# Performance work log

Measured on AMD Instinct MI355X. Metric: run time of the kernel, lower is better.

Reference implementation:

```python
import jax, jax.numpy as jnp
import numpy as np

NUM_CLASSES = 21
EPS = 1e-6
MOMENTUM = 0.99
K_WEAK = 16
K_STRONG = 256
PROB_THRESH = 0.95
IGNORE = 255
NEG = -1e30


def _normalize(x, axis=-1):
    # matches F.normalize(p=2) / CosineSimilarity with eps=1e-6
    n = jnp.linalg.norm(x, axis=axis, keepdims=True)
    return x / jnp.maximum(n, EPS)


def setup_inputs() -> dict:
    key = jax.random.key(0)
    k0, k1, k2, k3, k4, k5 = jax.random.split(key, 6)
    B, C, H, W = 8, 256, 128, 128
    feature_weak = jax.random.normal(k0, (B, C, H, W), jnp.float32)
    feature_strong = jax.random.normal(k1, (B, C, H, W), jnp.float32)
    probablity_weak = jax.random.uniform(k2, (B, H, W), jnp.float32)
    memory_bank = jax.random.normal(k3, (NUM_CLASSES, 1, C), jnp.float32)
    pred_weak = jax.random.randint(k4, (B, H, W), 0, NUM_CLASSES)
    ignore_mask = jax.random.randint(k5, (B, H, W), 0, 256)
    return {
        'feature_weak': feature_weak,
        'feature_strong': feature_strong,
        'probablity_weak': probablity_weak,
        'memory_bank': memory_bank,
        'pred_weak': pred_weak,
        'ignore_mask': ignore_mask,
    }


def reference(feature_weak, feature_strong, probablity_weak, memory_bank, pred_weak, ignore_mask):
    B, C, H, W = feature_weak.shape
    N = B * H * W
    fw = feature_weak.transpose(0, 2, 3, 1).reshape(N, C)   # weak pixel feats
    fs = feature_strong.transpose(0, 2, 3, 1).reshape(N, C) # strong pixel feats
    seg = pred_weak.reshape(N)
    ign = ignore_mask.reshape(N)  # same-size bilinear resize (align_corners) is identity
    prob = probablity_weak.reshape(N)

    valid = ign != IGNORE
    conf = valid & (prob > PROB_THRESH)

    cls = jnp.arange(NUM_CLASSES)
    is_cls = seg[None, :] == cls[:, None]        # [K, N]
    m_weak = is_cls & conf[None, :]              # per-class high-confidence mask
    m_strong = is_cls & valid[None, :]
    n_weak = m_weak.sum(axis=1)                  # [K]
    n_strong = m_strong.sum(axis=1)

    protos = memory_bank[:, 0, :]                # [K, C]
    pn = _normalize(protos)
    sim_w = _normalize(fw) @ pn.T                # [N, K] cos(pixel_weak, proto)
    sim_s = _normalize(fs) @ pn.T                # [N, K] cos(pixel_strong, proto)

    sw = jnp.where(m_weak, sim_w.T, NEG)         # [K, N]
    ss = jnp.where(m_strong, -sim_s.T, NEG)      # negate -> bottom-k via top_k
    _, idx_w = jax.lax.top_k(sw, K_WEAK)         # [K, 16] most-similar weak pixels
    _, idx_s = jax.lax.top_k(ss, K_STRONG)       # [K, 256] least-similar strong pixels

    # select_feature duplicates the top element: slots are ranks [0,0,1,...,14]
    ranks = jnp.maximum(jnp.arange(K_WEAK) - 1, 0)
    sel_w = fw[idx_w[:, ranks]]                  # [K, 16, C]
    sel_s = fs[idx_s]                            # [K, 256, C]

    kw = jnp.minimum(K_WEAK, n_weak)
    ks = jnp.minimum(K_STRONG, n_strong)
    valid_w = jnp.arange(K_WEAK)[None, :] < kw[:, None]     # [K, 16]
    valid_s = jnp.arange(K_STRONG)[None, :] < ks[:, None]   # [K, 256]

    # calculate_loss: weak side detached, max over strong dim, sum / strong count
    wn = _normalize(jax.lax.stop_gradient(sel_w))
    sn = _normalize(sel_s)
    cosm = jnp.einsum('kwc,ksc->kws', wn, sn)    # [K, 16, 256]
    cosm = jnp.where(valid_s[:, None, :], cosm, NEG)
    max_sim = jnp.where(valid_w, cosm.max(axis=2), 0.0)     # [K, 16]
    class_ok = (n_weak > 0) & (n_strong > 0)
    sim_sum = jnp.where(class_ok, max_sim.sum(axis=1), 0.0).sum()
    count = jnp.where(class_ok, ks, 0).sum()
    loss = jnp.where(count > 0, 1.0 - sim_sum / count, 0.0)

    # update_memory: per-class mean of high-confidence weak feats, EMA scatter
    fw_ng = jax.lax.stop_gradient(fw)            # .data copy -> no grad
    wsum = m_weak.astype(fw.dtype) @ fw_ng       # [K, C] segmented sum
    mean = wsum / jnp.maximum(n_weak, 1).astype(fw.dtype)[:, None]
    new_protos = jnp.where((n_weak > 0)[:, None],
                           MOMENTUM * protos + (1.0 - MOMENTUM) * mean,
                           protos)
    new_memory_bank = new_protos[:, None, :]     # [K, 1, C]
    return loss, new_memory_bank
```

## Files before the change

kernel.cpp:

```cpp
#include <hip/hip_runtime.h>
#include <stdint.h>

#define NCLS  21
#define CDIM  256
#define HWSZ  16384
#define NPIX  131072
#define EPSV  1e-6f
#define NEGV  -1e30f
#define CAP_W 4096
#define CAP_S 16384
#define KSEL  256
#define NCC   8
#define CCH   (CDIM/NCC)
#define NPART 8
#define NBLK  (NPIX/1024)

__device__ __forceinline__ uint64_t pack_key(float v, unsigned idx) {
  unsigned u = __float_as_uint(v);
  u = (u & 0x80000000u) ? ~u : (u | 0x80000000u);
  return ((uint64_t)(~u) << 32) | (uint64_t)idx;
}

__global__ void k0_init(const float* __restrict__ mb, float* pn, float* wsum) {
  int k = blockIdx.x, t = threadIdx.x;
  float v = mb[k * CDIM + t];
  float s = v * v;
  for (int o = 32; o > 0; o >>= 1) s += __shfl_down(s, o, 64);
  __shared__ float wsh[4];
  int wid = t >> 6, lane = t & 63;
  if (lane == 0) wsh[wid] = s;
  __syncthreads();
  float tot = wsh[0] + wsh[1] + wsh[2] + wsh[3];
  float inv = 1.0f / fmaxf(sqrtf(tot), EPSV);
  pn[k * CDIM + t] = v * inv;
  wsum[k * CDIM + t] = 0.0f;
}

__global__ void k1a_stream(const float* __restrict__ fw, const float* __restrict__ fs,
                           const float* __restrict__ prob, const int* __restrict__ seg,
                           const int* __restrict__ ign, const float* __restrict__ pn,
                           float* part, float* wsum, int* cnts) {
  __shared__ float pnT[CCH * NCLS];
  __shared__ float wloc[NCLS * (CCH + 1)];
  __shared__ int hs[NCLS], hw2[NCLS];
  int t = threadIdx.x;
  int pg = blockIdx.x;
  int cc = blockIdx.y;
  int c0 = cc * CCH;
  for (int i = t; i < CCH * NCLS; i += 256) {
    int c = i / NCLS, k = i % NCLS;
    pnT[i] = pn[k * CDIM + c0 + c];
  }
  for (int i = t; i < NCLS * (CCH + 1); i += 256) wloc[i] = 0.0f;
  if (cc == 0) {
    for (int i = t; i < NCLS; i += 256) { hs[i] = 0; hw2[i] = 0; }
  }
  __syncthreads();

  int n0 = pg * 1024 + t * 4;
  int b = n0 >> 14, hw = n0 & (HWSZ - 1);
  int4   sg = *(const int4*)(seg + n0);
  int4   ig = *(const int4*)(ign + n0);
  float4 pr = *(const float4*)(prob + n0);
  bool v0 = (ig.x != 255), v1 = (ig.y != 255), v2 = (ig.z != 255), v3 = (ig.w != 255);
  bool cf0 = v0 && (pr.x > 0.95f);
  bool cf1 = v1 && (pr.y > 0.95f);
  bool cf2 = v2 && (pr.z > 0.95f);
  bool cf3 = v3 && (pr.w > 0.95f);
  if (cc == 0) {
    if (v0) atomicAdd(&hs[sg.x], 1);
    if (v1) atomicAdd(&hs[sg.y], 1);
    if (v2) atomicAdd(&hs[sg.z], 1);
    if (v3) atomicAdd(&hs[sg.w], 1);
    if (cf0) atomicAdd(&hw2[sg.x], 1);
    if (cf1) atomicAdd(&hw2[sg.y], 1);
    if (cf2) atomicAdd(&hw2[sg.z], 1);
    if (cf3) atomicAdd(&hw2[sg.w], 1);
  }

  const float* fwp = fw + ((size_t)b * CDIM + c0) * HWSZ + hw;
  const float* fsp = fs + ((size_t)b * CDIM + c0) * HWSZ + hw;

  float4 dw = {0,0,0,0}, nw = {0,0,0,0}, dsv = {0,0,0,0}, ns = {0,0,0,0};
#pragma unroll 4
  for (int cl = 0; cl < CCH; ++cl) {
    float4 a = *(const float4*)(fwp + (size_t)cl * HWSZ);
    float4 s = *(const float4*)(fsp + (size_t)cl * HWSZ);
    float p0 = pnT[cl * NCLS + sg.x];
    float p1 = pnT[cl * NCLS + sg.y];
    float p2 = pnT[cl * NCLS + sg.z];
    float p3 = pnT[cl * NCLS + sg.w];
    dw.x = fmaf(a.x, p0, dw.x); nw.x = fmaf(a.x, a.x, nw.x);
    dw.y = fmaf(a.y, p1, dw.y); nw.y = fmaf(a.y, a.y, nw.y);
    dw.z = fmaf(a.z, p2, dw.z); nw.z = fmaf(a.z, a.z, nw.z);
    dw.w = fmaf(a.w, p3, dw.w); nw.w = fmaf(a.w, a.w, nw.w);
    dsv.x = fmaf(s.x, p0, dsv.x); ns.x = fmaf(s.x, s.x, ns.x);
    dsv.y = fmaf(s.y, p1, dsv.y); ns.y = fmaf(s.y, s.y, ns.y);
    dsv.z = fmaf(s.z, p2, dsv.z); ns.z = fmaf(s.z, s.z, ns.z);
    dsv.w = fmaf(s.w, p3, dsv.w); ns.w = fmaf(s.w, s.w, ns.w);
    if (cf0) atomicAdd(&wloc[sg.x * (CCH + 1) + cl], a.x);
    if (cf1) atomicAdd(&wloc[sg.y * (CCH + 1) + cl], a.y);
    if (cf2) atomicAdd(&wloc[sg.z * (CCH + 1) + cl], a.z);
    if (cf3) atomicAdd(&wloc[sg.w * (CCH + 1) + cl], a.w);
  }
  float4* pp = (float4*)part + ((size_t)cc * NPIX + n0);
  pp[0] = make_float4(dw.x, nw.x, dsv.x, ns.x);
  pp[1] = make_float4(dw.y, nw.y, dsv.y, ns.y);
  pp[2] = make_float4(dw.z, nw.z, dsv.z, ns.z);
  pp[3] = make_float4(dw.w, nw.w, dsv.w, ns.w);

  __syncthreads();
  for (int i = t; i < NCLS * CCH; i += 256) {
    int k = i / CCH, cl = i % CCH;
    float v = wloc[k * (CCH + 1) + cl];
    if (v != 0.0f) atomicAdd(&wsum[k * CDIM + c0 + cl], v);
  }
  if (cc == 0) {
    for (int i = t; i < NCLS; i += 256) {
      cnts[pg * NCLS + i] = hs[i];
      cnts[NBLK * NCLS + pg * NCLS + i] = hw2[i];
    }
  }
}

__global__ void ks_scan(const int* __restrict__ cnts, int* offs, int* scnt, int* wcnt) {
  __shared__ int L[2 * NBLK * NCLS];
  int t = threadIdx.x;
  for (int i = t; i < 2 * NBLK * NCLS; i += 256) L[i] = cnts[i];
  __syncthreads();
  if (t < 2 * NCLS) {
    int q = t % NCLS;
    int typ = t / NCLS;
    int base = typ * NBLK * NCLS;
    int run = 0;
    for (int b2 = 0; b2 < NBLK; ++b2) {
      int v = L[base + b2 * NCLS + q];
      L[base + b2 * NCLS + q] = run;
      run += v;
    }
    if (typ == 0) scnt[q] = run; else wcnt[q] = run;
  }
  __syncthreads();
  for (int i = t; i < 2 * NBLK * NCLS; i += 256) offs[i] = L[i];
}

__global__ void k1b_write(const float* __restrict__ part, const float* __restrict__ prob,
                          const int* __restrict__ seg, const int* __restrict__ ign,
                          const int* __restrict__ offs, uint64_t* wkeys, uint64_t* skeys) {
  __shared__ int ls[NCLS], lw[NCLS];
  int t = threadIdx.x, pg = blockIdx.x;
  if (t < NCLS) {
    ls[t] = offs[pg * NCLS + t];
    lw[t] = offs[NBLK * NCLS + pg * NCLS + t];
  }
  __syncthreads();
  int n0 = pg * 1024 + t * 4;
  int4   sg = *(const int4*)(seg + n0);
  int4   ig = *(const int4*)(ign + n0);
  float4 pr = *(const float4*)(prob + n0);
  float dw[4] = {0,0,0,0}, nw[4] = {0,0,0,0}, ds[4] = {0,0,0,0}, ns[4] = {0,0,0,0};
#pragma unroll
  for (int cc = 0; cc < NCC; ++cc) {
    const float4* pp = (const float4*)part + ((size_t)cc * NPIX + n0);
#pragma unroll
    for (int i = 0; i < 4; ++i) {
      float4 v = pp[i];
      dw[i] += v.x; nw[i] += v.y; ds[i] += v.z; ns[i] += v.w;
    }
  }
  int   sga[4] = {sg.x, sg.y, sg.z, sg.w};
  int   iga[4] = {ig.x, ig.y, ig.z, ig.w};
  float pra[4] = {pr.x, pr.y, pr.z, pr.w};
#pragma unroll
  for (int i = 0; i < 4; ++i) {
    if (iga[i] != 255) {
      int q = sga[i];
      float sim_s = ds[i] / fmaxf(sqrtf(ns[i]), EPSV);
      int pos = atomicAdd(&ls[q], 1);
      if (pos < CAP_S) skeys[(size_t)q * CAP_S + pos] = pack_key(-sim_s, (unsigned)(n0 + i));
      if (pra[i] > 0.95f) {
        float sim_w = dw[i] / fmaxf(sqrtf(nw[i]), EPSV);
        int pw = atomicAdd(&lw[q], 1);
        if (pw < CAP_W) wkeys[(size_t)q * CAP_W + pw] = pack_key(sim_w, (unsigned)(n0 + i));
      }
    }
  }
}

__device__ void select_topk(const uint64_t* __restrict__ list, int cnt,
                            uint64_t* T, uint64_t* P, int* pcnt, int* woff) {
  int t = threadIdx.x;
  T[t] = ~0ull;
  if (t == 0) *pcnt = 0;
  __syncthreads();
  for (int base = 0; base < cnt; base += 256) {
    uint64_t key = (base + t < cnt) ? list[base + t] : ~0ull;
    uint64_t cutoff = T[KSEL - 1];
    bool pred = key < cutoff;
    unsigned long long mask = __ballot(pred);
    int wid = t >> 6, lane = t & 63;
    if (lane == 0) woff[wid] = __popcll(mask);
    int prefix = __popcll(mask & ((1ull << lane) - 1ull));
    __syncthreads();
    int off = 0;
    for (int w2 = 0; w2 < wid; ++w2) off += woff[w2];
    int total = woff[0] + woff[1] + woff[2] + woff[3];
    int old = *pcnt;
    if (pred) P[old + off + prefix] = key;
    int newc = old + total;
    __syncthreads();
    if (t == 0) *pcnt = newc;
    bool last = (base + 256 >= cnt);
    if (newc >= KSEL || (last && newc > 0)) {
      for (int i2 = t; i2 < 2 * KSEL; i2 += 256)
        if (i2 >= newc) P[i2] = ~0ull;
      for (unsigned size = 2; size <= 2 * KSEL; size <<= 1) {
        for (unsigned stride = size >> 1; stride > 0; stride >>= 1) {
          __syncthreads();
          unsigned lo = stride - 1;
          unsigned i = (((unsigned)t & ~lo) << 1) | ((unsigned)t & lo);
          unsigned j = i | stride;
          uint64_t a = P[i], b = P[j];
          bool up = ((i & size) == 0);
          if ((a > b) == up) { P[i] = b; P[j] = a; }
        }
      }
      __syncthreads();
      uint64_t a = T[t], b = P[KSEL - 1 - t];
      T[t] = a < b ? a : b;
      for (unsigned stride = KSEL / 2; stride > 0; stride >>= 1) {
        __syncthreads();
        if (((unsigned)t & stride) == 0) {
          uint64_t x = T[t], y = T[t + stride];
          if (x > y) { T[t] = y; T[t + stride] = x; }
        }
      }
      __syncthreads();
      if (t == 0) *pcnt = 0;
      __syncthreads();
    } else {
      __syncthreads();
    }
  }
}

__global__ void k2_topk(const uint64_t* __restrict__ wkeys, const uint64_t* __restrict__ skeys,
                        const int* wcnt, const int* scnt,
                        uint64_t* psel, int* idxw, int* kwv, int* nwv) {
  __shared__ uint64_t T[KSEL];
  __shared__ uint64_t P[2 * KSEL];
  __shared__ int pcnt;
  __shared__ int woff[4];
  int bid = blockIdx.x, t = threadIdx.x;
  if (bid < NCLS * NPART) {
    int k = bid / NPART, p = bid % NPART;
    int cnt = min(scnt[k], CAP_S);
    int chunk = (cnt + NPART - 1) / NPART;
    int lo = p * chunk;
    int hi = min(lo + chunk, cnt);
    int c = hi > lo ? hi - lo : 0;
    select_topk(skeys + (size_t)k * CAP_S + lo, c, T, P, &pcnt, woff);
    psel[((size_t)k * NPART + p) * KSEL + t] = T[t];
  } else {
    int k = bid - NCLS * NPART;
    int cnt_total = wcnt[k];
    int cnt = min(cnt_total, CAP_W);
    select_topk(wkeys + (size_t)k * CAP_W, cnt, T, P, &pcnt, woff);
    if (t < 16) idxw[k * 16 + t] = (int)(unsigned)(T[t] & 0xFFFFFFFFull);
    if (t == 0) { nwv[k] = cnt_total; kwv[k] = min(cnt_total, 16); }
  }
}

__global__ void k2m_merge(const uint64_t* __restrict__ psel, const int* scnt,
                          int* idxs, int* ksv, int* nsv) {
  int k = blockIdx.x, t = threadIdx.x;
  __shared__ uint64_t M[NPART * KSEL];
  for (int i = t; i < NPART * KSEL; i += 256) M[i] = psel[(size_t)k * NPART * KSEL + i];
  for (unsigned size = 2; size <= NPART * KSEL; size <<= 1) {
    for (unsigned stride = size >> 1; stride > 0; stride >>= 1) {
      __syncthreads();
      for (unsigned q = t; q < NPART * KSEL / 2; q += 256) {
        unsigned lo = stride - 1;
        unsigned i = ((q & ~lo) << 1) | (q & lo);
        unsigned j = i | stride;
        uint64_t a = M[i], b = M[j];
        bool up = ((i & size) == 0);
        if ((a > b) == up) { M[i] = b; M[j] = a; }
      }
    }
  }
  __syncthreads();
  idxs[k * KSEL + t] = (int)(unsigned)(M[t] & 0xFFFFFFFFull);
  if (t == 0) { int c = scnt[k]; nsv[k] = c; ksv[k] = c < KSEL ? c : KSEL; }
}

__global__ void k3a_gather(const float* __restrict__ fw, const float* __restrict__ fs,
                           const int* __restrict__ idxw, const int* __restrict__ idxs,
                           const int* __restrict__ kwv, const int* __restrict__ ksv,
                           float* dw_dense, float* ds_dense) {
  int k = blockIdx.y;
  int slot = blockIdx.x;
  int t = threadIdx.x;
  bool strong = slot < KSEL;
  float v = 0.0f;
  int n = 0;
  bool ok;
  if (strong) {
    ok = slot < ksv[k];
    if (ok) n = idxs[k * KSEL + slot];
  } else {
    int i = slot - KSEL;
    ok = i < kwv[k];
    int rank = i > 0 ? i - 1 : 0;
    if (ok) n = idxw[k * 16 + rank];
  }
  if (ok) {
    int b = n >> 14, hw = n & (HWSZ - 1);
    const float* f = strong ? fs : fw;
    v = f[(size_t)(b * CDIM + t) * HWSZ + hw];
  }
  float s = v * v;
  for (int o = 32; o > 0; o >>= 1) s += __shfl_down(s, o, 64);
  __shared__ float wsh[4];
  int wid = t >> 6, lane = t & 63;
  if (lane == 0) wsh[wid] = s;
  __syncthreads();
  float tot = wsh[0] + wsh[1] + wsh[2] + wsh[3];
  float inv = 1.0f / fmaxf(sqrtf(tot), EPSV);
  float out = v * inv;
  if (strong) ds_dense[((size_t)k * KSEL + slot) * CDIM + t] = out;
  else        dw_dense[((size_t)k * 16 + (slot - KSEL)) * CDIM + t] = out;
}

__global__ void k3b_loss(const float* __restrict__ dw_dense, const float* __restrict__ ds_dense,
                         const int* kwv, const int* ksv, const int* nwv, const int* nsv,
                         float* simsum, int* countk) {
  int k = blockIdx.x, t = threadIdx.x;
  int wid = t >> 6, lane = t & 63;
  __shared__ float wn[16 * CDIM];
  __shared__ float wred[4][16];
  for (int i = t; i < 16 * CDIM; i += 256) wn[i] = dw_dense[(size_t)k * 16 * CDIM + i];
  __syncthreads();
  int ks_ = ksv[k], kw_ = kwv[k];
  bool ok = (nwv[k] > 0) && (nsv[k] > 0);
  float dots[16];
#pragma unroll
  for (int i = 0; i < 16; ++i) dots[i] = 0.0f;
  bool jv = ok && (t < ks_);
  if (jv) {
    const float4* sp = (const float4*)(ds_dense + ((size_t)k * KSEL + t) * CDIM);
    for (int c4 = 0; c4 < CDIM / 4; ++c4) {
      float4 v = sp[c4];
#pragma unroll
      for (int i = 0; i < 16; ++i) {
        float4 w = ((const float4*)(wn + i * CDIM))[c4];
        dots[i] = fmaf(v.x, w.x, dots[i]);
        dots[i] = fmaf(v.y, w.y, dots[i]);
        dots[i] = fmaf(v.z, w.z, dots[i]);
        dots[i] = fmaf(v.w, w.w, dots[i]);
      }
    }
  }
#pragma unroll
  for (int i = 0; i < 16; ++i) {
    float v = jv ? dots[i] : NEGV;
    for (int o = 32; o > 0; o >>= 1) v = fmaxf(v, __shfl_down(v, o, 64));
    if (lane == 0) wred[wid][i] = v;
  }
  __syncthreads();
  if (t == 0) {
    float csum = 0.0f;
    for (int i = 0; i < kw_; ++i) {
      float m = fmaxf(fmaxf(wred[0][i], wred[1][i]), fmaxf(wred[2][i], wred[3][i]));
      csum += m;
    }
    simsum[k] = ok ? csum : 0.0f;
    countk[k] = ok ? ks_ : 0;
  }
}

__global__ void k4_final(const float* __restrict__ mb, const float* __restrict__ wsum,
                         const int* __restrict__ nwv, const float* __restrict__ simsum,
                         const int* __restrict__ countk, float* out) {
  int k = blockIdx.x, t = threadIdx.x;
  float p = mb[k * CDIM + t];
  float o = p;
  int nw = nwv[k];
  if (nw > 0) {
    float mean = wsum[k * CDIM + t] / (float)nw;
    o = 0.99f * p + 0.01f * mean;
  }
  out[1 + k * CDIM + t] = o;
  if (k == 0 && t == 0) {
    float ss = 0.0f;
    int cc = 0;
    for (int q = 0; q < NCLS; ++q) { ss += simsum[q]; cc += countk[q]; }
    out[0] = (cc > 0) ? (1.0f - ss / (float)cc) : 0.0f;
  }
}

extern "C" void kernel_launch(void* const* d_in, const int* in_sizes, int n_in,
                              void* d_out, int out_size, void* d_ws, size_t ws_size,
                              hipStream_t stream) {
  const float* fw   = (const float*)d_in[0];
  const float* fs   = (const float*)d_in[1];
  const float* prob = (const float*)d_in[2];
  const float* mb   = (const float*)d_in[3];
  const int*   seg  = (const int*)d_in[4];
  const int*   ign  = (const int*)d_in[5];
  float* out = (float*)d_out;

  char* ws = (char*)d_ws;
  size_t off = 0;
  auto alloc = [&](size_t bytes) -> char* {
    char* p = ws + off;
    off = (off + bytes + 255) & ~(size_t)255;
    return p;
  };
  float*    pn       = (float*)alloc(NCLS * CDIM * 4);
  float*    wsum     = (float*)alloc(NCLS * CDIM * 4);
  int*      wcnt     = (int*)alloc(NCLS * 4);
  int*      scnt     = (int*)alloc(NCLS * 4);
  int*      idxw     = (int*)alloc(NCLS * 16 * 4);
  int*      idxs     = (int*)alloc(NCLS * KSEL * 4);
  int*      kwv      = (int*)alloc(NCLS * 4);
  int*      ksv      = (int*)alloc(NCLS * 4);
  int*      nwv      = (int*)alloc(NCLS * 4);
  int*      nsv      = (int*)alloc(NCLS * 4);
  float*    simsum   = (float*)alloc(NCLS * 4);
  int*      countk   = (int*)alloc(NCLS * 4);
  int*      cnts     = (int*)alloc(2 * NBLK * NCLS * 4);
  int*      offs     = (int*)alloc(2 * NBLK * NCLS * 4);
  uint64_t* wkeys    = (uint64_t*)alloc((size_t)NCLS * CAP_W * 8);
  uint64_t* skeys    = (uint64_t*)alloc((size_t)NCLS * CAP_S * 8);
  uint64_t* psel     = (uint64_t*)alloc((size_t)NCLS * NPART * KSEL * 8);
  float*    dw_dense = (float*)alloc((size_t)NCLS * 16 * CDIM * 4);
  float*    ds_dense = (float*)alloc((size_t)NCLS * KSEL * CDIM * 4);
  float*    part     = (float*)alloc((size_t)NCC * NPIX * 4 * 4);
  (void)in_sizes; (void)n_in; (void)out_size; (void)ws_size;

  k0_init<<<NCLS, 256, 0, stream>>>(mb, pn, wsum);
  k1a_stream<<<dim3(NBLK, NCC), 256, 0, stream>>>(fw, fs, prob, seg, ign, pn,
                                                  part, wsum, cnts);
  ks_scan<<<1, 256, 0, stream>>>(cnts, offs, scnt, wcnt);
  k1b_write<<<NBLK, 256, 0, stream>>>(part, prob, seg, ign, offs, wkeys, skeys);
  k2_topk<<<NCLS * NPART + NCLS, 256, 0, stream>>>(wkeys, skeys, wcnt, scnt,
                                                   psel, idxw, kwv, nwv);
  k2m_merge<<<NCLS, 256, 0, stream>>>(psel, scnt, idxs, ksv, nsv);
  k3a_gather<<<dim3(KSEL + 16, NCLS), 256, 0, stream>>>(fw, fs, idxw, idxs, kwv, ksv,
                                                        dw_dense, ds_dense);
  k3b_loss<<<NCLS, 256, 0, stream>>>(dw_dense, ds_dense, kwv, ksv, nwv, nsv,
                                     simsum, countk);
  k4_final<<<NCLS, 256, 0, stream>>>(mb, wsum, nwv, simsum, countk, out);
}
```

Baseline: 431.8 us.

## Move segmented weak-feature sum out of streaming kernel into gather over selected keys

Removes the per-channel shared-memory atomics that accumulated the confident weak features inside the main streaming kernel. A new kernel does the same sum by gathering features through the indices already written to the weak key lists. The streaming kernel also now handles 2 pixels per thread (512 per block) instead of 4, and the gather kernel handles 4 slots per block. The new path adds strided gathers of about 5% of pixels and relies on the weak key lists being complete, so classes that exceed CAP_W would drop entries from the sum.

```diff
diff --git a/kernel.cpp b/kernel.cpp
--- a/kernel.cpp
+++ b/kernel.cpp
@@ -13,7 +13,8 @@
 #define NCC   8
 #define CCH   (CDIM/NCC)
 #define NPART 8
-#define NBLK  (NPIX/1024)
+#define NBLK2 (NPIX/512)
+#define WPAR  8
 
 __device__ __forceinline__ uint64_t pack_key(float v, unsigned idx) {
   unsigned u = __float_as_uint(v);
@@ -39,9 +40,8 @@
 __global__ void k1a_stream(const float* __restrict__ fw, const float* __restrict__ fs,
                            const float* __restrict__ prob, const int* __restrict__ seg,
                            const int* __restrict__ ign, const float* __restrict__ pn,
-                           float* part, float* wsum, int* cnts) {
+                           float* part, int* cnts) {
   __shared__ float pnT[CCH * NCLS];
-  __shared__ float wloc[NCLS * (CCH + 1)];
   __shared__ int hs[NCLS], hw2[NCLS];
   int t = threadIdx.x;
   int pg = blockIdx.x;
@@ -51,89 +51,63 @@
     int c = i / NCLS, k = i % NCLS;
     pnT[i] = pn[k * CDIM + c0 + c];
   }
-  for (int i = t; i < NCLS * (CCH + 1); i += 256) wloc[i] = 0.0f;
   if (cc == 0) {
     for (int i = t; i < NCLS; i += 256) { hs[i] = 0; hw2[i] = 0; }
   }
   __syncthreads();
 
-  int n0 = pg * 1024 + t * 4;
+  int n0 = pg * 512 + t * 2;
   int b = n0 >> 14, hw = n0 & (HWSZ - 1);
-  int4   sg = *(const int4*)(seg + n0);
-  int4   ig = *(const int4*)(ign + n0);
-  float4 pr = *(const float4*)(prob + n0);
-  bool v0 = (ig.x != 255), v1 = (ig.y != 255), v2 = (ig.z != 255), v3 = (ig.w != 255);
-  bool cf0 = v0 && (pr.x > 0.95f);
-  bool cf1 = v1 && (pr.y > 0.95f);
-  bool cf2 = v2 && (pr.z > 0.95f);
-  bool cf3 = v3 && (pr.w > 0.95f);
+  int2   sg = *(const int2*)(seg + n0);
+  int2   ig = *(const int2*)(ign + n0);
+  float2 pr = *(const float2*)(prob + n0);
   if (cc == 0) {
+    bool v0 = (ig.x != 255), v1 = (ig.y != 255);
     if (v0) atomicAdd(&hs[sg.x], 1);
     if (v1) atomicAdd(&hs[sg.y], 1);
-    if (v2) atomicAdd(&hs[sg.z], 1);
-    if (v3) atomicAdd(&hs[sg.w], 1);
-    if (cf0) atomicAdd(&hw2[sg.x], 1);
-    if (cf1) atomicAdd(&hw2[sg.y], 1);
-    if (cf2) atomicAdd(&hw2[sg.z], 1);
-    if (cf3) atomicAdd(&hw2[sg.w], 1);
+    if (v0 && pr.x > 0.95f) atomicAdd(&hw2[sg.x], 1);
+    if (v1 && pr.y > 0.95f) atomicAdd(&hw2[sg.y], 1);
   }
 
   const float* fwp = fw + ((size_t)b * CDIM + c0) * HWSZ + hw;
   const float* fsp = fs + ((size_t)b * CDIM + c0) * HWSZ + hw;
 
-  float4 dw = {0,0,0,0}, nw = {0,0,0,0}, dsv = {0,0,0,0}, ns = {0,0,0,0};
-#pragma unroll 4
+  float2 dw = {0,0}, nw = {0,0}, dsv = {0,0}, ns = {0,0};
+#pragma unroll 8
   for (int cl = 0; cl < CCH; ++cl) {
-    float4 a = *(const float4*)(fwp + (size_t)cl * HWSZ);
-    float4 s = *(const float4*)(fsp + (size_t)cl * HWSZ);
+    float2 a = *(const float2*)(fwp + (size_t)cl * HWSZ);
+    float2 s = *(const float2*)(fsp + (size_t)cl * HWSZ);
     float p0 = pnT[cl * NCLS + sg.x];
     float p1 = pnT[cl * NCLS + sg.y];
-    float p2 = pnT[cl * NCLS + sg.z];
-    float p3 = pnT[cl * NCLS + sg.w];
     dw.x = fmaf(a.x, p0, dw.x); nw.x = fmaf(a.x, a.x, nw.x);
     dw.y = fmaf(a.y, p1, dw.y); nw.y = fmaf(a.y, a.y, nw.y);
-    dw.z = fmaf(a.z, p2, dw.z); nw.z = fmaf(a.z, a.z, nw.z);
-    dw.w = fmaf(a.w, p3, dw.w); nw.w = fmaf(a.w, a.w, nw.w);
     dsv.x = fmaf(s.x, p0, dsv.x); ns.x = fmaf(s.x, s.x, ns.x);
     dsv.y = fmaf(s.y, p1, dsv.y); ns.y = fmaf(s.y, s.y, ns.y);
-    dsv.z = fmaf(s.z, p2, dsv.z); ns.z = fmaf(s.z, s.z, ns.z);
-    dsv.w = fmaf(s.w, p3, dsv.w); ns.w = fmaf(s.w, s.w, ns.w);
-    if (cf0) atomicAdd(&wloc[sg.x * (CCH + 1) + cl], a.x);
-    if (cf1) atomicAdd(&wloc[sg.y * (CCH + 1) + cl], a.y);
-    if (cf2) atomicAdd(&wloc[sg.z * (CCH + 1) + cl], a.z);
-    if (cf3) atomicAdd(&wloc[sg.w * (CCH + 1) + cl], a.w);
   }
   float4* pp = (float4*)part + ((size_t)cc * NPIX + n0);
   pp[0] = make_float4(dw.x, nw.x, dsv.x, ns.x);
   pp[1] = make_float4(dw.y, nw.y, dsv.y, ns.y);
-  pp[2] = make_float4(dw.z, nw.z, dsv.z, ns.z);
-  pp[3] = make_float4(dw.w, nw.w, dsv.w, ns.w);
-
-  __syncthreads();
-  for (int i = t; i < NCLS * CCH; i += 256) {
-    int k = i / CCH, cl = i % CCH;
-    float v = wloc[k * (CCH + 1) + cl];
-    if (v != 0.0f) atomicAdd(&wsum[k * CDIM + c0 + cl], v);
-  }
+
   if (cc == 0) {
+    __syncthreads();
     for (int i = t; i < NCLS; i += 256) {
       cnts[pg * NCLS + i] = hs[i];
-      cnts[NBLK * NCLS + pg * NCLS + i] = hw2[i];
+      cnts[NBLK2 * NCLS + pg * NCLS + i] = hw2[i];
     }
   }
 }
 
 __global__ void ks_scan(const int* __restrict__ cnts, int* offs, int* scnt, int* wcnt) {
-  __shared__ int L[2 * NBLK * NCLS];
+  __shared__ int L[2 * NBLK2 * NCLS];
   int t = threadIdx.x;
-  for (int i = t; i < 2 * NBLK * NCLS; i += 256) L[i] = cnts[i];
+  for (int i = t; i < 2 * NBLK2 * NCLS; i += 256) L[i] = cnts[i];
   __syncthreads();
   if (t < 2 * NCLS) {
     int q = t % NCLS;
     int typ = t / NCLS;
-    int base = typ * NBLK * NCLS;
+    int base = typ * NBLK2 * NCLS;
     int run = 0;
-    for (int b2 = 0; b2 < NBLK; ++b2) {
+    for (int b2 = 0; b2 < NBLK2; ++b2) {
       int v = L[base + b2 * NCLS + q];
       L[base + b2 * NCLS + q] = run;
       run += v;
@@ -141,7 +115,7 @@
     if (typ == 0) scnt[q] = run; else wcnt[q] = run;
   }
   __syncthreads();
-  for (int i = t; i < 2 * NBLK * NCLS; i += 256) offs[i] = L[i];
+  for (int i = t; i < 2 * NBLK2 * NCLS; i += 256) offs[i] = L[i];
 }
 
 __global__ void k1b_write(const float* __restrict__ part, const float* __restrict__ prob,
@@ -151,28 +125,28 @@
   int t = threadIdx.x, pg = blockIdx.x;
   if (t < NCLS) {
     ls[t] = offs[pg * NCLS + t];
-    lw[t] = offs[NBLK * NCLS + pg * NCLS + t];
-  }
-  __syncthreads();
-  int n0 = pg * 1024 + t * 4;
-  int4   sg = *(const int4*)(seg + n0);
-  int4   ig = *(const int4*)(ign + n0);
-  float4 pr = *(const float4*)(prob + n0);
-  float dw[4] = {0,0,0,0}, nw[4] = {0,0,0,0}, ds[4] = {0,0,0,0}, ns[4] = {0,0,0,0};
+    lw[t] = offs[NBLK2 * NCLS + pg * NCLS + t];
+  }
+  __syncthreads();
+  int n0 = pg * 512 + t * 2;
+  int2   sg = *(const int2*)(seg + n0);
+  int2   ig = *(const int2*)(ign + n0);
+  float2 pr = *(const float2*)(prob + n0);
+  float dw[2] = {0,0}, nw[2] = {0,0}, ds[2] = {0,0}, ns[2] = {0,0};
 #pragma unroll
   for (int cc = 0; cc < NCC; ++cc) {
     const float4* pp = (const float4*)part + ((size_t)cc * NPIX + n0);
 #pragma unroll
-    for (int i = 0; i < 4; ++i) {
+    for (int i = 0; i < 2; ++i) {
       float4 v = pp[i];
       dw[i] += v.x; nw[i] += v.y; ds[i] += v.z; ns[i] += v.w;
     }
   }
-  int   sga[4] = {sg.x, sg.y, sg.z, sg.w};
-  int   iga[4] = {ig.x, ig.y, ig.z, ig.w};
-  float pra[4] = {pr.x, pr.y, pr.z, pr.w};
-#pragma unroll
-  for (int i = 0; i < 4; ++i) {
+  int   sga[2] = {sg.x, sg.y};
+  int   iga[2] = {ig.x, ig.y};
+  float pra[2] = {pr.x, pr.y};
+#pragma unroll
+  for (int i = 0; i < 2; ++i) {
     if (iga[i] != 255) {
       int q = sga[i];
       float sim_s = ds[i] / fmaxf(sqrtf(ns[i]), EPSV);
@@ -185,6 +159,19 @@
       }
     }
   }
+}
+
+__global__ void kw_sum(const float* __restrict__ fw, const uint64_t* __restrict__ wkeys,
+                       const int* __restrict__ wcnt, float* wsum) {
+  int k = blockIdx.x, p = blockIdx.y, t = threadIdx.x;
+  int cnt = min(wcnt[k], CAP_W);
+  float acc = 0.0f;
+  for (int i = p; i < cnt; i += WPAR) {
+    unsigned idx = (unsigned)(wkeys[(size_t)k * CAP_W + i] & 0xFFFFFFFFull);
+    int b = idx >> 14, hw = idx & (HWSZ - 1);
+    acc += fw[((size_t)(b * CDIM) + t) * HWSZ + hw];
+  }
+  if (acc != 0.0f) atomicAdd(&wsum[k * CDIM + t], acc);
 }
 
 __device__ void select_topk(const uint64_t* __restrict__ list, int cnt,
@@ -299,37 +286,55 @@
                            const int* __restrict__ kwv, const int* __restrict__ ksv,
                            float* dw_dense, float* ds_dense) {
   int k = blockIdx.y;
-  int slot = blockIdx.x;
+  int s0 = blockIdx.x * 4;
   int t = threadIdx.x;
-  bool strong = slot < KSEL;
-  float v = 0.0f;
-  int n = 0;
-  bool ok;
-  if (strong) {
-    ok = slot < ksv[k];
-    if (ok) n = idxs[k * KSEL + slot];
-  } else {
-    int i = slot - KSEL;
-    ok = i < kwv[k];
-    int rank = i > 0 ? i - 1 : 0;
-    if (ok) n = idxw[k * 16 + rank];
-  }
-  if (ok) {
-    int b = n >> 14, hw = n & (HWSZ - 1);
-    const float* f = strong ? fs : fw;
-    v = f[(size_t)(b * CDIM + t) * HWSZ + hw];
-  }
-  float s = v * v;
-  for (int o = 32; o > 0; o >>= 1) s += __shfl_down(s, o, 64);
-  __shared__ float wsh[4];
   int wid = t >> 6, lane = t & 63;
-  if (lane == 0) wsh[wid] = s;
-  __syncthreads();
-  float tot = wsh[0] + wsh[1] + wsh[2] + wsh[3];
-  float inv = 1.0f / fmaxf(sqrtf(tot), EPSV);
-  float out = v * inv;
-  if (strong) ds_dense[((size_t)k * KSEL + slot) * CDIM + t] = out;
-  else        dw_dense[((size_t)k * 16 + (slot - KSEL)) * CDIM + t] = out;
+  float v[4];
+  bool strong[4];
+  int slot_[4];
+#pragma unroll
+  for (int j = 0; j < 4; ++j) {
+    int slot = s0 + j;
+    slot_[j] = slot;
+    strong[j] = slot < KSEL;
+    bool ok;
+    int n = 0;
+    if (strong[j]) {
+      ok = slot < ksv[k];
+      if (ok) n = idxs[k * KSEL + slot];
+    } else {
+      int i = slot - KSEL;
+      ok = i < kwv[k];
+      int rank = i > 0 ? i - 1 : 0;
+      if (ok) n = idxw[k * 16 + rank];
+    }
+    v[j] = 0.0f;
+    if (ok) {
+      int b = n >> 14, hw = n & (HWSZ - 1);
+      const float* f = strong[j] ? fs : fw;
+      v[j] = f[(size_t)(b * CDIM + t) * HWSZ + hw];
+    }
+  }
+  __shared__ float wsh[4][4];
+  float s[4];
+#pragma unroll
+  for (int j = 0; j < 4; ++j) {
+    s[j] = v[j] * v[j];
+    for (int o = 32; o > 0; o >>= 1) s[j] += __shfl_down(s[j], o, 64);
+  }
+  if (lane == 0) {
+#pragma unroll
+    for (int j = 0; j < 4; ++j) wsh[wid][j] = s[j];
+  }
+  __syncthreads();
+#pragma unroll
+  for (int j = 0; j < 4; ++j) {
+    float tot = wsh[0][j] + wsh[1][j] + wsh[2][j] + wsh[3][j];
+    float inv = 1.0f / fmaxf(sqrtf(tot), EPSV);
+    float out = v[j] * inv;
+    if (strong[j]) ds_dense[((size_t)k * KSEL + slot_[j]) * CDIM + t] = out;
+    else           dw_dense[((size_t)k * 16 + (slot_[j] - KSEL)) * CDIM + t] = out;
+  }
 }
 
 __global__ void k3b_loss(const float* __restrict__ dw_dense, const float* __restrict__ ds_dense,
@@ -429,8 +434,8 @@
   int*      nsv      = (int*)alloc(NCLS * 4);
   float*    simsum   = (float*)alloc(NCLS * 4);
   int*      countk   = (int*)alloc(NCLS * 4);
-  int*      cnts     = (int*)alloc(2 * NBLK * NCLS * 4);
-  int*      offs     = (int*)alloc(2 * NBLK * NCLS * 4);
+  int*      cnts     = (int*)alloc(2 * NBLK2 * NCLS * 4);
+  int*      offs     = (int*)alloc(2 * NBLK2 * NCLS * 4);
   uint64_t* wkeys    = (uint64_t*)alloc((size_t)NCLS * CAP_W * 8);
   uint64_t* skeys    = (uint64_t*)alloc((size_t)NCLS * CAP_S * 8);
   uint64_t* psel     = (uint64_t*)alloc((size_t)NCLS * NPART * KSEL * 8);
@@ -440,15 +445,16 @@
   (void)in_sizes; (void)n_in; (void)out_size; (void)ws_size;
 
   k0_init<<<NCLS, 256, 0, stream>>>(mb, pn, wsum);
-  k1a_stream<<<dim3(NBLK, NCC), 256, 0, stream>>>(fw, fs, prob, seg, ign, pn,
-                                                  part, wsum, cnts);
+  k1a_stream<<<dim3(NBLK2, NCC), 256, 0, stream>>>(fw, fs, prob, seg, ign, pn,
+                                                   part, cnts);
   ks_scan<<<1, 256, 0, stream>>>(cnts, offs, scnt, wcnt);
-  k1b_write<<<NBLK, 256, 0, stream>>>(part, prob, seg, ign, offs, wkeys, skeys);
+  k1b_write<<<NBLK2, 256, 0, stream>>>(part, prob, seg, ign, offs, wkeys, skeys);
+  kw_sum<<<dim3(NCLS, WPAR), 256, 0, stream>>>(fw, wkeys, wcnt, wsum);
   k2_topk<<<NCLS * NPART + NCLS, 256, 0, stream>>>(wkeys, skeys, wcnt, scnt,
                                                    psel, idxw, kwv, nwv);
   k2m_merge<<<NCLS, 256, 0, stream>>>(psel, scnt, idxs, ksv, nsv);
-  k3a_gather<<<dim3(KSEL + 16, NCLS), 256, 0, stream>>>(fw, fs, idxw, idxs, kwv, ksv,
-                                                        dw_dense, ds_dense);
+  k3a_gather<<<dim3((KSEL + 16) / 4, NCLS), 256, 0, stream>>>(fw, fs, idxw, idxs, kwv, ksv,
+                                                              dw_dense, ds_dense);
   k3b_loss<<<NCLS, 256, 0, stream>>>(dw_dense, ds_dense, kwv, ksv, nwv, nsv,
                                      simsum, countk);
   k4_final<<<NCLS, 256, 0, stream>>>(mb, wsum, nwv, simsum, countk, out);
```

Result: slower. 460.0 us (+6.5%).
